# Kernel optimization log

Measured on AMD Instinct MI355X. Metric: run time of the kernel, lower is better.

Reference implementation:

```python
import jax, jax.numpy as jnp
import numpy as np

B, S, D, E, HD, F, L, CYCLES = 2, 1024, 1000, 20, 50, 2048, 14, 3


def setup_inputs() -> dict:
    key = jax.random.key(0)
    k = jax.random.split(key, 8)
    sc = 0.02
    return {
        "x": jax.random.normal(k[0], (B, S, D), jnp.float32),
        "expert_w": jax.random.normal(k[1], (L, E, D, 3 * HD), jnp.float32) * sc,
        "expert_b": jnp.zeros((L, E, 3 * HD), jnp.float32),
        "router_w": jax.random.normal(k[2], (L, D, E), jnp.float32) * sc,
        "router_b": jnp.zeros((L, E), jnp.float32),
        "out_w": jax.random.normal(k[3], (L, D, D), jnp.float32) * sc,
        "out_b": jnp.zeros((L, D), jnp.float32),
        "ln1_g": jnp.ones((L, D), jnp.float32),
        "ln1_b": jnp.zeros((L, D), jnp.float32),
        "ff_w1": jax.random.normal(k[4], (L, D, F), jnp.float32) * sc,
        "ff_b1": jnp.zeros((L, F), jnp.float32),
        "ff_w2": jax.random.normal(k[5], (L, F, D), jnp.float32) * sc,
        "ff_b2": jnp.zeros((L, D), jnp.float32),
        "ln2_g": jnp.ones((L, D), jnp.float32),
        "ln2_b": jnp.zeros((L, D), jnp.float32),
    }


def _layer_norm(x, g, b):
    m = jnp.mean(x, -1, keepdims=True)
    v = jnp.mean((x - m) ** 2, -1, keepdims=True)
    return (x - m) * jax.lax.rsqrt(v + 1e-5) * g + b


def _moe_attn(x, ew, eb, rw, rb, ow, ob):
    # x: [b, s, d]; ew: [E, d, 3*HD]; routing softmax over experts
    b_, s_, d_ = x.shape
    routing = jax.nn.softmax(x @ rw + rb, axis=-1)           # [b, s, E]
    qkv = jnp.einsum('bsd,edh->besh', x, ew) + eb[None, :, None, :]
    q, k, v = jnp.split(qkv, 3, axis=-1)                     # each [b, E, s, HD]
    scores = jnp.einsum('besh,beth->best', q, k) * (HD ** -0.5)
    attn = jax.nn.softmax(scores, axis=-1)
    out = jnp.einsum('best,beth->besh', attn, v)             # [b, E, s, HD]
    out = out * jnp.transpose(routing, (0, 2, 1))[..., None]
    # disjoint head slices -> reshape is exactly the torch slice-add combine
    out = jnp.transpose(out, (0, 2, 1, 3)).reshape(b_, s_, d_)
    return out @ ow + ob


def _block(x, i, p):
    a = _moe_attn(x, p['expert_w'][i], p['expert_b'][i], p['router_w'][i],
                  p['router_b'][i], p['out_w'][i], p['out_b'][i])
    x = _layer_norm(x + a, p['ln1_g'][i], p['ln1_b'][i])
    h = jax.nn.gelu(x @ p['ff_w1'][i] + p['ff_b1'][i], approximate=False)
    f = h @ p['ff_w2'][i] + p['ff_b2'][i]
    return _layer_norm(x + f, p['ln2_g'][i], p['ln2_b'][i])


def _slam(x, p):
    s = x.shape[1]
    x = _block(x, 0, p)
    bounds = [(0, min(int(s * 0.45), s)),
              (max(int(s * 0.25), 0), min(int(s * 0.65), s)),
              (max(int(s * 0.45), 0), min(int(s * 0.85), s)),
              (max(int(s * 0.65), 0), s)]
    wrap = max(min(int(s * 0.05), s // 10), 1) if s > 20 else 0
    counts = np.zeros(s, np.float32)
    for st, en in bounds:
        counts[st:en] += 1.0
    if wrap:
        counts[:wrap] += 1.0
    counts = jnp.asarray(np.maximum(counts, 1.0))[None, :, None]
    for c in range(CYCLES):
        x_new = jnp.zeros_like(x)
        for j, (st, en) in enumerate(bounds):
            li = 1 + 4 * c + j
            if j == 3 and wrap:
                seg = jnp.concatenate([x[:, st:s], x[:, :wrap]], axis=1)
                out = _block(seg, li, p)
                x_new = x_new.at[:, st:s].add(out[:, :s - st])
                x_new = x_new.at[:, :wrap].add(out[:, s - st:])
            else:
                out = _block(x[:, st:en], li, p)
                x_new = x_new.at[:, st:en].add(out)
        x = x_new / counts
    return _block(x, L - 1, p)


def reference(x, expert_w, expert_b, router_w, router_b, out_w, out_b,
              ln1_g, ln1_b, ff_w1, ff_b1, ff_w2, ff_b2, ln2_g, ln2_b):
    p = dict(expert_w=expert_w, expert_b=expert_b, router_w=router_w,
             router_b=router_b, out_w=out_w, out_b=out_b, ln1_g=ln1_g,
             ln1_b=ln1_b, ff_w1=ff_w1, ff_b1=ff_b1, ff_w2=ff_w2,
             ff_b2=ff_b2, ln2_g=ln2_g, ln2_b=ln2_b)
    return _slam(x, p)
```

## Files before the change

kernel.cpp:

```cpp
#include <hip/hip_runtime.h>
#include <math.h>

namespace {

constexpr int kB  = 2;
constexpr int kS  = 1024;
constexpr int kD  = 1000;
constexpr int kE  = 20;
constexpr int kHD = 50;
constexpr int kF  = 2048;
constexpr int kQKV = 3 * kHD;

__global__ __launch_bounds__(256) void zero_kernel(float* __restrict__ p, int n) {
    int i = blockIdx.x * 256 + threadIdx.x;
    if (i < n) p[i] = 0.0f;
}

__global__ __launch_bounds__(256) void gelu_kernel(float* __restrict__ p, int n) {
    int i = blockIdx.x * 256 + threadIdx.x;
    if (i < n) {
        float x = p[i];
        p[i] = 0.5f * x * (1.0f + erff(x * 0.70710678118654752440f));
    }
}

__global__ __launch_bounds__(256) void init_bias_kernel(float* __restrict__ C,
                                                        const float* __restrict__ bias,
                                                        long long total, int N) {
    long long i = (long long)blockIdx.x * 256 + threadIdx.x;
    if (i < total) C[i] = bias[(int)(i % N)];
}

__global__ __launch_bounds__(256) void gather_kernel(const float* __restrict__ src,
                                                     float* __restrict__ dst,
                                                     int st, int sseg) {
    int i = blockIdx.x * 256 + threadIdx.x;
    int tot = kB * sseg * kD;
    if (i >= tot) return;
    int d  = i % kD;
    int tr = i / kD;
    int r  = tr % sseg;
    int b  = tr / sseg;
    int srow = st + r;
    if (srow >= kS) srow -= kS;
    dst[i] = src[(b * kS + srow) * kD + d];
}

__global__ __launch_bounds__(256) void scatter_add_kernel(const float* __restrict__ src,
                                                          float* __restrict__ dst,
                                                          int st, int sseg) {
    int i = blockIdx.x * 256 + threadIdx.x;
    int tot = kB * sseg * kD;
    if (i >= tot) return;
    int d  = i % kD;
    int tr = i / kD;
    int r  = tr % sseg;
    int b  = tr / sseg;
    int drow = st + r;
    if (drow >= kS) drow -= kS;
    dst[(b * kS + drow) * kD + d] += src[i];
}

__global__ __launch_bounds__(256) void finalize_kernel(const float* __restrict__ xn,
                                                       float* __restrict__ cur) {
    int i = blockIdx.x * 256 + threadIdx.x;
    const int tot = kB * kS * kD;
    if (i >= tot) return;
    int r = (i / kD) % kS;
    float cnt = 0.0f;
    cnt += (r < 460) ? 1.0f : 0.0f;
    cnt += (r >= 256 && r < 665) ? 1.0f : 0.0f;
    cnt += (r >= 460 && r < 870) ? 1.0f : 0.0f;
    cnt += (r >= 665) ? 1.0f : 0.0f;
    cnt += (r < 51) ? 1.0f : 0.0f;
    cnt = fmaxf(cnt, 1.0f);
    cur[i] = xn[i] / cnt;
}

template<int BM, int BN, int TM, int TN, int NMAP, bool ATOMIC>
__global__ __launch_bounds__(256) void gemm_tile(
    const float* __restrict__ A, const float* __restrict__ W,
    const float* __restrict__ bias, float* __restrict__ C,
    int M, int N, int K, int kchunk,
    long long strideW, long long strideC, long long strideBias)
{
    constexpr int BK = 16;
    constexpr int TX = BN / TN;
    constexpr int TY = BM / TM;
    static_assert(TX * TY == 256, "block must be 256 threads");
    static_assert(TM % 4 == 0 && TN % 4 == 0, "vector frags");

    int kbeg = 0, kend = K;
    if (ATOMIC) {
        kbeg = blockIdx.z * kchunk;
        kend = min(K, kbeg + kchunk);
    } else {
        W    += (long long)blockIdx.z * strideW;
        C    += (long long)blockIdx.z * strideC;
        bias += (long long)blockIdx.z * strideBias;
    }

    __shared__ __align__(16) float As[BK][BM + 4];
    __shared__ __align__(16) float Bs[BK][BN];

    const int tid  = threadIdx.x;
    const int tx   = tid % TX;
    const int ty   = tid / TX;
    const int row0 = blockIdx.y * BM;
    const int col0 = blockIdx.x * BN;

    float acc[TM][TN] = {};

    for (int k0 = kbeg; k0 < kend; k0 += BK) {
        #pragma unroll
        for (int i = 0; i < BM / 64; i++) {
            int f  = tid + i * 256;
            int r  = f >> 2;
            int cv = f & 3;
            int gr = row0 + r;
            int gc = k0 + cv * 4;
            float4 av = make_float4(0.f, 0.f, 0.f, 0.f);
            if (gr < M) {
                if (gc + 3 < kend) {
                    av = *reinterpret_cast<const float4*>(A + (long long)gr * K + gc);
                } else {
                    float t0 = (gc + 0 < kend) ? A[(long long)gr * K + gc + 0] : 0.f;
                    float t1 = (gc + 1 < kend) ? A[(long long)gr * K + gc + 1] : 0.f;
                    float t2 = (gc + 2 < kend) ? A[(long long)gr * K + gc + 2] : 0.f;
                    float t3 = (gc + 3 < kend) ? A[(long long)gr * K + gc + 3] : 0.f;
                    av = make_float4(t0, t1, t2, t3);
                }
            }
            As[cv * 4 + 0][r] = av.x;
            As[cv * 4 + 1][r] = av.y;
            As[cv * 4 + 2][r] = av.z;
            As[cv * 4 + 3][r] = av.w;
        }

        if (NMAP > 0) {
            #pragma unroll
            for (int it = 0; it < (BK * BN) / 256; it++) {
                int idx = tid + it * 256;
                int r = idx / BN, c = idx % BN;
                int gr = k0 + r, gc = col0 + c;
                float v = 0.f;
                if (gr < kend && gc < N) {
                    int e = gc / NMAP;
                    int n = gc - e * NMAP;
                    v = W[(long long)e * K * NMAP + (long long)gr * NMAP + n];
                }
                Bs[r][c] = v;
            }
        } else {
            #pragma unroll
            for (int i = 0; i < BN / 64; i++) {
                int f  = tid + i * 256;
                int r  = f / (BN / 4);
                int cv = f % (BN / 4);
                int gr = k0 + r;
                int gc = col0 + cv * 4;
                float4 bv = make_float4(0.f, 0.f, 0.f, 0.f);
                if (gr < kend) {
                    if (gc + 3 < N) {
                        bv = *reinterpret_cast<const float4*>(W + (long long)gr * N + gc);
                    } else {
                        float t0 = (gc + 0 < N) ? W[(long long)gr * N + gc + 0] : 0.f;
                        float t1 = (gc + 1 < N) ? W[(long long)gr * N + gc + 1] : 0.f;
                        float t2 = (gc + 2 < N) ? W[(long long)gr * N + gc + 2] : 0.f;
                        float t3 = (gc + 3 < N) ? W[(long long)gr * N + gc + 3] : 0.f;
                        bv = make_float4(t0, t1, t2, t3);
                    }
                }
                *reinterpret_cast<float4*>(&Bs[r][cv * 4]) = bv;
            }
        }
        __syncthreads();

        #pragma unroll
        for (int kk = 0; kk < BK; kk++) {
            float a[TM], b[TN];
            #pragma unroll
            for (int i = 0; i < TM; i += 4) {
                float4 v = *reinterpret_cast<const float4*>(&As[kk][ty * TM + i]);
                a[i] = v.x; a[i + 1] = v.y; a[i + 2] = v.z; a[i + 3] = v.w;
            }
            #pragma unroll
            for (int j = 0; j < TN; j += 4) {
                float4 v = *reinterpret_cast<const float4*>(&Bs[kk][tx * TN + j]);
                b[j] = v.x; b[j + 1] = v.y; b[j + 2] = v.z; b[j + 3] = v.w;
            }
            #pragma unroll
            for (int i = 0; i < TM; i++)
                #pragma unroll
                for (int j = 0; j < TN; j++)
                    acc[i][j] = fmaf(a[i], b[j], acc[i][j]);
        }
        __syncthreads();
    }

    #pragma unroll
    for (int i = 0; i < TM; i++) {
        int gr = row0 + ty * TM + i;
        if (gr >= M) continue;
        if (ATOMIC) {
            #pragma unroll
            for (int j = 0; j < TN; j++) {
                int gc = col0 + tx * TN + j;
                if (gc < N) atomicAdd(&C[(long long)gr * N + gc], acc[i][j]);
            }
        } else if (NMAP > 0) {
            #pragma unroll
            for (int j = 0; j < TN; j++) {
                int gc = col0 + tx * TN + j;
                if (gc < N) {
                    int e = gc / NMAP;
                    int n = gc - e * NMAP;
                    C[(long long)e * M * NMAP + (long long)gr * NMAP + n] =
                        acc[i][j] + bias[gc];
                }
            }
        } else {
            #pragma unroll
            for (int j = 0; j < TN; j += 4) {
                int gc = col0 + tx * TN + j;
                if (gc + 3 < N) {
                    float4 bv = *reinterpret_cast<const float4*>(bias + gc);
                    float4 o  = make_float4(acc[i][j + 0] + bv.x,
                                            acc[i][j + 1] + bv.y,
                                            acc[i][j + 2] + bv.z,
                                            acc[i][j + 3] + bv.w);
                    *reinterpret_cast<float4*>(C + (long long)gr * N + gc) = o;
                } else {
                    for (int jj = 0; jj < 4; jj++) {
                        int g = gc + jj;
                        if (g < N) C[(long long)gr * N + g] = acc[i][j + jj] + bias[g];
                    }
                }
            }
        }
    }
}

inline int pick_split(int gx, int gy, int K) {
    int blocks = gx * gy;
    int S = (512 + blocks - 1) / blocks;
    if (S < 1) S = 1;
    if (S > 4) S = 4;
    while (S > 1 && (K + S - 1) / S < 64) S--;
    return S;
}

inline void gemm_auto(const float* A, const float* W, const float* bias, float* C,
                      int M, int N, int K, hipStream_t stream)
{
    constexpr int BM = 128, BN = 64, TM = 8, TN = 4;
    int gx = (N + BN - 1) / BN, gy = (M + BM - 1) / BM;
    int S = pick_split(gx, gy, K);
    if (S == 1) {
        dim3 grid(gx, gy, 1);
        gemm_tile<BM, BN, TM, TN, 0, false><<<grid, 256, 0, stream>>>(
            A, W, bias, C, M, N, K, K, 0, 0, 0);
    } else {
        long long total = (long long)M * N;
        init_bias_kernel<<<(unsigned)((total + 255) / 256), 256, 0, stream>>>(
            C, bias, total, N);
        int Kc = ((K + S - 1) / S + 15) & ~15;
        dim3 grid(gx, gy, S);
        gemm_tile<BM, BN, TM, TN, 0, true><<<grid, 256, 0, stream>>>(
            A, W, nullptr, C, M, N, K, Kc, 0, 0, 0);
    }
}

__global__ __launch_bounds__(256) void routing_kernel(
    const float* __restrict__ X, const float* __restrict__ RW,
    const float* __restrict__ RB, float* __restrict__ R, int T)
{
    int wave = (blockIdx.x * 256 + threadIdx.x) / 64;
    int lane = threadIdx.x & 63;
    if (wave >= T) return;
    const float* x = X + (long long)wave * kD;

    float xr[16];
    #pragma unroll
    for (int i = 0; i < 16; i++) {
        int d = lane + 64 * i;
        xr[i] = (d < kD) ? x[d] : 0.0f;
    }
    float r[kE];
    #pragma unroll
    for (int e = 0; e < kE; e++) {
        float acc = 0.0f;
        #pragma unroll
        for (int i = 0; i < 16; i++) {
            int d = lane + 64 * i;
            if (d < kD) acc = fmaf(xr[i], RW[d * kE + e], acc);
        }
        #pragma unroll
        for (int off = 32; off > 0; off >>= 1) acc += __shfl_xor(acc, off, 64);
        r[e] = acc + RB[e];
    }
    float m = r[0];
    #pragma unroll
    for (int e = 1; e < kE; e++) m = fmaxf(m, r[e]);
    float sum = 0.0f;
    #pragma unroll
    for (int e = 0; e < kE; e++) { r[e] = expf(r[e] - m); sum += r[e]; }
    float inv = 1.0f / sum;
    float mine = 0.0f;
    #pragma unroll
    for (int e = 0; e < kE; e++) if (lane == e) mine = r[e] * inv;
    if (lane < kE) R[(long long)wave * kE + lane] = mine;
}

constexpr int QT_STR = 68;
constexpr int VS_STR = 52;
constexpr int SB_STR = 68;

__global__ __launch_bounds__(256) void attn_kernel(
    const float* __restrict__ QKV, const float* __restrict__ R,
    float* __restrict__ O, int s)
{
    const int q0 = blockIdx.x * 64;
    const int e  = blockIdx.y;
    const int b  = blockIdx.z;
    const int T  = kB * s;
    const float* base = QKV + ((long long)e * T + (long long)b * s) * kQKV;

    __shared__ __align__(16) float Qt[kHD * QT_STR];
    __shared__ __align__(16) float Vs[64 * VS_STR];
    __shared__ __align__(16) float KS[64 * SB_STR];

    const int tid = threadIdx.x;
    const int tx  = tid & 15;
    const int ty  = tid >> 4;
    const int row = ty * 4;

    for (int idx = tid; idx < 64 * kHD; idx += 256) {
        int r = idx / kHD, h = idx % kHD;
        int q = q0 + r;
        Qt[h * QT_STR + r] = (q < s) ? base[(long long)q * kQKV + h] : 0.0f;
    }

    float o[4][4] = {};
    float m[4] = {-1e30f, -1e30f, -1e30f, -1e30f};
    float l[4] = {};

    const int ntile = (s + 63) / 64;
    for (int t = 0; t < ntile; t++) {
        const int k0 = t * 64;
        const int kn = min(64, s - k0);

        __syncthreads();
        for (int idx = tid; idx < 64 * kHD; idx += 256) {
            int r = idx / kHD, h = idx % kHD;
            const float* rowp = base + (long long)(k0 + r) * kQKV;
            bool ok = (r < kn);
            KS[h * SB_STR + r]  = ok ? rowp[kHD + h] : 0.0f;
            Vs[r * VS_STR + h]  = ok ? rowp[2 * kHD + h] : 0.0f;
        }
        __syncthreads();

        float sacc[4][4] = {};
        #pragma unroll 2
        for (int kk = 0; kk < kHD; kk++) {
            float4 a4 = *reinterpret_cast<const float4*>(&Qt[kk * QT_STR + row]);
            float4 b4 = *reinterpret_cast<const float4*>(&KS[kk * SB_STR + tx * 4]);
            const float av[4] = {a4.x, a4.y, a4.z, a4.w};
            const float bv[4] = {b4.x, b4.y, b4.z, b4.w};
            #pragma unroll
            for (int i = 0; i < 4; i++)
                #pragma unroll
                for (int j = 0; j < 4; j++)
                    sacc[i][j] = fmaf(av[i], bv[j], sacc[i][j]);
        }

        #pragma unroll
        for (int i = 0; i < 4; i++) {
            #pragma unroll
            for (int j = 0; j < 4; j++) {
                float v = sacc[i][j] * 0.14142135623730950488f;
                sacc[i][j] = (tx * 4 + j < kn) ? v : -1e30f;
            }
            float rm = fmaxf(fmaxf(sacc[i][0], sacc[i][1]),
                             fmaxf(sacc[i][2], sacc[i][3]));
            rm = fmaxf(rm, __shfl_xor(rm, 1, 64));
            rm = fmaxf(rm, __shfl_xor(rm, 2, 64));
            rm = fmaxf(rm, __shfl_xor(rm, 4, 64));
            rm = fmaxf(rm, __shfl_xor(rm, 8, 64));
            float mn = fmaxf(m[i], rm);
            float alpha = __expf(m[i] - mn);
            m[i] = mn;
            float rs = 0.0f;
            #pragma unroll
            for (int j = 0; j < 4; j++) {
                float p = __expf(sacc[i][j] - mn);
                sacc[i][j] = p;
                rs += p;
            }
            rs += __shfl_xor(rs, 1, 64);
            rs += __shfl_xor(rs, 2, 64);
            rs += __shfl_xor(rs, 4, 64);
            rs += __shfl_xor(rs, 8, 64);
            l[i] = l[i] * alpha + rs;
            #pragma unroll
            for (int c = 0; c < 4; c++) o[i][c] *= alpha;
        }

        __syncthreads();
        #pragma unroll
        for (int i = 0; i < 4; i++)
            *reinterpret_cast<float4*>(&KS[(row + i) * SB_STR + tx * 4]) =
                make_float4(sacc[i][0], sacc[i][1], sacc[i][2], sacc[i][3]);
        __syncthreads();

        #pragma unroll 2
        for (int j0 = 0; j0 < 64; j0 += 4) {
            float4 pr[4], vr[4];
            #pragma unroll
            for (int i = 0; i < 4; i++)
                pr[i] = *reinterpret_cast<const float4*>(&KS[(row + i) * SB_STR + j0]);
            #pragma unroll
            for (int jj = 0; jj < 4; jj++)
                vr[jj] = *reinterpret_cast<const float4*>(&Vs[(j0 + jj) * VS_STR + tx * 4]);
            #pragma unroll
            for (int i = 0; i < 4; i++) {
                const float pv[4] = {pr[i].x, pr[i].y, pr[i].z, pr[i].w};
                #pragma unroll
                for (int jj = 0; jj < 4; jj++) {
                    o[i][0] = fmaf(pv[jj], vr[jj].x, o[i][0]);
                    o[i][1] = fmaf(pv[jj], vr[jj].y, o[i][1]);
                    o[i][2] = fmaf(pv[jj], vr[jj].z, o[i][2]);
                    o[i][3] = fmaf(pv[jj], vr[jj].w, o[i][3]);
                }
            }
        }
    }

    const int hbase = tx * 4;
    if (hbase < kHD) {
        #pragma unroll
        for (int i = 0; i < 4; i++) {
            int q = q0 + row + i;
            if (q >= s) continue;
            long long tok = (long long)b * s + q;
            float sc = R[tok * kE + e] / l[i];
            float* op = O + tok * kD + e * kHD + hbase;
            if (hbase + 3 < kHD) {
                *reinterpret_cast<float2*>(op) =
                    make_float2(o[i][0] * sc, o[i][1] * sc);
                *reinterpret_cast<float2*>(op + 2) =
                    make_float2(o[i][2] * sc, o[i][3] * sc);
            } else {
                op[0] = o[i][0] * sc;
                op[1] = o[i][1] * sc;
            }
        }
    }
}

__global__ __launch_bounds__(256) void ln_kernel(
    const float* __restrict__ Xres, const float* __restrict__ A,
    const float* __restrict__ G, const float* __restrict__ Bb,
    float* __restrict__ Y)
{
    const int t = blockIdx.x;
    const float* x = Xres + (long long)t * kD;
    const float* a = A + (long long)t * kD;
    __shared__ float buf[kD];
    __shared__ float red[4];
    const int tid = threadIdx.x;

    float lsum = 0.0f;
    for (int d = tid; d < kD; d += 256) {
        float v = x[d] + a[d];
        buf[d] = v;
        lsum += v;
    }
    #pragma unroll
    for (int off = 32; off > 0; off >>= 1) lsum += __shfl_xor(lsum, off, 64);
    if ((tid & 63) == 0) red[tid >> 6] = lsum;
    __syncthreads();
    float mean = (red[0] + red[1] + red[2] + red[3]) * (1.0f / kD);

    float lv = 0.0f;
    for (int d = tid; d < kD; d += 256) {
        float u = buf[d] - mean;
        lv = fmaf(u, u, lv);
    }
    #pragma unroll
    for (int off = 32; off > 0; off >>= 1) lv += __shfl_xor(lv, off, 64);
    __syncthreads();
    if ((tid & 63) == 0) red[tid >> 6] = lv;
    __syncthreads();
    float var = (red[0] + red[1] + red[2] + red[3]) * (1.0f / kD);
    float inv = rsqrtf(var + 1e-5f);

    for (int d = tid; d < kD; d += 256)
        Y[(long long)t * kD + d] = (buf[d] - mean) * inv * G[d] + Bb[d];
}

struct Params {
    const float *expert_w, *expert_b, *router_w, *router_b, *out_w, *out_b;
    const float *ln1_g, *ln1_b, *ff_w1, *ff_b1, *ff_w2, *ff_b2, *ln2_g, *ln2_b;
};

void run_block(const float* xin, float* xout, int s, int li, const Params& P,
               float* routing, float* qkv, float* attn_comb, float* a_out,
               float* y1, float* h, float* f, hipStream_t stream)
{
    const int T = kB * s;

    routing_kernel<<<(T + 3) / 4, 256, 0, stream>>>(
        xin, P.router_w + (long long)li * kD * kE, P.router_b + li * kE, routing, T);

    {
        dim3 grid((kE * kQKV + 63) / 64, (T + 127) / 128, 1);
        gemm_tile<128, 64, 8, 4, kQKV, false><<<grid, 256, 0, stream>>>(
            xin, P.expert_w + (long long)li * kE * kD * kQKV,
            P.expert_b + (long long)li * kE * kQKV, qkv,
            T, kE * kQKV, kD, kD, 0, 0, 0);
    }

    {
        dim3 grid((s + 63) / 64, kE, kB);
        attn_kernel<<<grid, 256, 0, stream>>>(qkv, routing, attn_comb, s);
    }

    gemm_auto(attn_comb, P.out_w + (long long)li * kD * kD,
              P.out_b + li * kD, a_out, T, kD, kD, stream);

    ln_kernel<<<T, 256, 0, stream>>>(xin, a_out, P.ln1_g + li * kD, P.ln1_b + li * kD, y1);

    gemm_auto(y1, P.ff_w1 + (long long)li * kD * kF,
              P.ff_b1 + li * kF, h, T, kF, kD, stream);

    gelu_kernel<<<(T * kF + 255) / 256, 256, 0, stream>>>(h, T * kF);

    gemm_auto(h, P.ff_w2 + (long long)li * kF * kD,
              P.ff_b2 + li * kD, f, T, kD, kF, stream);

    ln_kernel<<<T, 256, 0, stream>>>(y1, f, P.ln2_g + li * kD, P.ln2_b + li * kD, xout);
}

}

extern "C" void kernel_launch(void* const* d_in, const int* in_sizes, int n_in,
                              void* d_out, int out_size, void* d_ws, size_t ws_size,
                              hipStream_t stream)
{
    const float* x = (const float*)d_in[0];
    Params P;
    P.expert_w = (const float*)d_in[1];
    P.expert_b = (const float*)d_in[2];
    P.router_w = (const float*)d_in[3];
    P.router_b = (const float*)d_in[4];
    P.out_w    = (const float*)d_in[5];
    P.out_b    = (const float*)d_in[6];
    P.ln1_g    = (const float*)d_in[7];
    P.ln1_b    = (const float*)d_in[8];
    P.ff_w1    = (const float*)d_in[9];
    P.ff_b1    = (const float*)d_in[10];
    P.ff_w2    = (const float*)d_in[11];
    P.ff_b2    = (const float*)d_in[12];
    P.ln2_g    = (const float*)d_in[13];
    P.ln2_b    = (const float*)d_in[14];

    const int TD = kB * kS * kD;
    float* ws = (float*)d_ws;
    float* cur       = ws;  ws += TD;
    float* xnew      = ws;  ws += TD;
    float* seg       = ws;  ws += TD;
    float* routing   = ws;  ws += kB * kS * kE;
    float* qkv       = ws;  ws += kE * kB * kS * kQKV;
    float* attn_comb = ws;  ws += TD;
    float* a_out     = ws;  ws += TD;
    float* y1        = ws;  ws += TD;
    float* h         = ws;  ws += kB * kS * kF;
    float* f         = ws;  ws += TD;
    float* bout      = (float*)d_out;

    run_block(x, cur, kS, 0, P, routing, qkv, attn_comb, a_out, y1, h, f, stream);

    const int st_arr[4]  = {0, 256, 460, 665};
    const int len_arr[4] = {460, 409, 410, 410};

    for (int c = 0; c < 3; c++) {
        zero_kernel<<<(TD + 255) / 256, 256, 0, stream>>>(xnew, TD);
        for (int j = 0; j < 4; j++) {
            const int st = st_arr[j], sl = len_arr[j];
            const int li = 1 + 4 * c + j;
            const int n = kB * sl * kD;
            gather_kernel<<<(n + 255) / 256, 256, 0, stream>>>(cur, seg, st, sl);
            run_block(seg, bout, sl, li, P, routing, qkv, attn_comb, a_out, y1, h, f, stream);
            scatter_add_kernel<<<(n + 255) / 256, 256, 0, stream>>>(bout, xnew, st, sl);
        }
        finalize_kernel<<<(TD + 255) / 256, 256, 0, stream>>>(xnew, cur);
    }

    run_block(cur, (float*)d_out, kS, 13, P, routing, qkv, attn_comb, a_out, y1, h, f, stream);
}
```

Measured before the change: 10.56 ms.

## Double-buffer GEMM tiles, add 128x128 tile path, fuse GELU into FF1 epilogue

Rewrites the fp32 tiled GEMM to prefetch the next K-tile into registers and store it into a second shared-memory buffer while the current one is computed, so each K-step needs one barrier instead of two. The per-thread fragment is split into strided 4-wide groups to reduce LDS bank conflicts. A 128x128 tile variant is used when the grid is large enough, and the split-K heuristic is retuned. GELU is applied in the FF1 GEMM epilogue instead of a separate pass. In exchange, shared memory and register use go up, which may lower occupancy.

```diff
diff --git a/kernel.cpp b/kernel.cpp
--- a/kernel.cpp
+++ b/kernel.cpp
@@ -77,31 +77,27 @@
     cur[i] = xn[i] / cnt;
 }
 
-template<int BM, int BN, int TM, int TN, int NMAP, bool ATOMIC>
+template<int BM, int BN, int TM, int TN, int NMAP, bool ATOMIC, bool GELU>
 __global__ __launch_bounds__(256) void gemm_tile(
     const float* __restrict__ A, const float* __restrict__ W,
     const float* __restrict__ bias, float* __restrict__ C,
-    int M, int N, int K, int kchunk,
-    long long strideW, long long strideC, long long strideBias)
-{
-    constexpr int BK = 16;
-    constexpr int TX = BN / TN;
-    constexpr int TY = BM / TM;
+    int M, int N, int K, int kchunk)
+{
+    constexpr int BK  = 16;
+    constexpr int NGM = TM / 4;
+    constexpr int NGN = TN / 4;
+    constexpr int TX  = BN / TN;
+    constexpr int TY  = BM / TM;
     static_assert(TX * TY == 256, "block must be 256 threads");
-    static_assert(TM % 4 == 0 && TN % 4 == 0, "vector frags");
 
     int kbeg = 0, kend = K;
-    if (ATOMIC) {
+    if constexpr (ATOMIC) {
         kbeg = blockIdx.z * kchunk;
         kend = min(K, kbeg + kchunk);
-    } else {
-        W    += (long long)blockIdx.z * strideW;
-        C    += (long long)blockIdx.z * strideC;
-        bias += (long long)blockIdx.z * strideBias;
-    }
-
-    __shared__ __align__(16) float As[BK][BM + 4];
-    __shared__ __align__(16) float Bs[BK][BN];
+    }
+
+    __shared__ __align__(16) float As[2][BK][BM + 4];
+    __shared__ __align__(16) float Bs[2][BK][BN];
 
     const int tid  = threadIdx.x;
     const int tx   = tid % TX;
@@ -109,11 +105,19 @@
     const int row0 = blockIdx.y * BM;
     const int col0 = blockIdx.x * BN;
 
-    float acc[TM][TN] = {};
-
-    for (int k0 = kbeg; k0 < kend; k0 += BK) {
-        #pragma unroll
-        for (int i = 0; i < BM / 64; i++) {
+    constexpr int AV  = BM / 64;
+    constexpr int BV  = (NMAP == 0) ? BN / 64 : 1;
+    constexpr int BSC = (NMAP > 0) ? (BK * BN / 256) : 1;
+
+    float4 areg[AV];
+    float4 breg[BV];
+    float  bsc[BSC];
+
+    float acc[NGM][4][NGN][4] = {};
+
+    auto loadg = [&](int k0) {
+        #pragma unroll
+        for (int i = 0; i < AV; i++) {
             int f  = tid + i * 256;
             int r  = f >> 2;
             int cv = f & 3;
@@ -124,23 +128,18 @@
                 if (gc + 3 < kend) {
                     av = *reinterpret_cast<const float4*>(A + (long long)gr * K + gc);
                 } else {
-                    float t0 = (gc + 0 < kend) ? A[(long long)gr * K + gc + 0] : 0.f;
-                    float t1 = (gc + 1 < kend) ? A[(long long)gr * K + gc + 1] : 0.f;
-                    float t2 = (gc + 2 < kend) ? A[(long long)gr * K + gc + 2] : 0.f;
-                    float t3 = (gc + 3 < kend) ? A[(long long)gr * K + gc + 3] : 0.f;
-                    av = make_float4(t0, t1, t2, t3);
+                    av.x = (gc + 0 < kend) ? A[(long long)gr * K + gc + 0] : 0.f;
+                    av.y = (gc + 1 < kend) ? A[(long long)gr * K + gc + 1] : 0.f;
+                    av.z = (gc + 2 < kend) ? A[(long long)gr * K + gc + 2] : 0.f;
+                    av.w = (gc + 3 < kend) ? A[(long long)gr * K + gc + 3] : 0.f;
                 }
             }
-            As[cv * 4 + 0][r] = av.x;
-            As[cv * 4 + 1][r] = av.y;
-            As[cv * 4 + 2][r] = av.z;
-            As[cv * 4 + 3][r] = av.w;
-        }
-
-        if (NMAP > 0) {
-            #pragma unroll
-            for (int it = 0; it < (BK * BN) / 256; it++) {
-                int idx = tid + it * 256;
+            areg[i] = av;
+        }
+        if constexpr (NMAP > 0) {
+            #pragma unroll
+            for (int i = 0; i < BSC; i++) {
+                int idx = tid + i * 256;
                 int r = idx / BN, c = idx % BN;
                 int gr = k0 + r, gc = col0 + c;
                 float v = 0.f;
@@ -149,11 +148,11 @@
                     int n = gc - e * NMAP;
                     v = W[(long long)e * K * NMAP + (long long)gr * NMAP + n];
                 }
-                Bs[r][c] = v;
+                bsc[i] = v;
             }
         } else {
             #pragma unroll
-            for (int i = 0; i < BN / 64; i++) {
+            for (int i = 0; i < BV; i++) {
                 int f  = tid + i * 256;
                 int r  = f / (BN / 4);
                 int cv = f % (BN / 4);
@@ -164,76 +163,135 @@
                     if (gc + 3 < N) {
                         bv = *reinterpret_cast<const float4*>(W + (long long)gr * N + gc);
                     } else {
-                        float t0 = (gc + 0 < N) ? W[(long long)gr * N + gc + 0] : 0.f;
-                        float t1 = (gc + 1 < N) ? W[(long long)gr * N + gc + 1] : 0.f;
-                        float t2 = (gc + 2 < N) ? W[(long long)gr * N + gc + 2] : 0.f;
-                        float t3 = (gc + 3 < N) ? W[(long long)gr * N + gc + 3] : 0.f;
-                        bv = make_float4(t0, t1, t2, t3);
+                        bv.x = (gc + 0 < N) ? W[(long long)gr * N + gc + 0] : 0.f;
+                        bv.y = (gc + 1 < N) ? W[(long long)gr * N + gc + 1] : 0.f;
+                        bv.z = (gc + 2 < N) ? W[(long long)gr * N + gc + 2] : 0.f;
+                        bv.w = (gc + 3 < N) ? W[(long long)gr * N + gc + 3] : 0.f;
                     }
                 }
-                *reinterpret_cast<float4*>(&Bs[r][cv * 4]) = bv;
-            }
-        }
-        __syncthreads();
-
+                breg[i] = bv;
+            }
+        }
+    };
+
+    auto stlds = [&](int buf) {
+        #pragma unroll
+        for (int i = 0; i < AV; i++) {
+            int f  = tid + i * 256;
+            int r  = f >> 2;
+            int cv = f & 3;
+            As[buf][cv * 4 + 0][r] = areg[i].x;
+            As[buf][cv * 4 + 1][r] = areg[i].y;
+            As[buf][cv * 4 + 2][r] = areg[i].z;
+            As[buf][cv * 4 + 3][r] = areg[i].w;
+        }
+        if constexpr (NMAP > 0) {
+            #pragma unroll
+            for (int i = 0; i < BSC; i++) {
+                int idx = tid + i * 256;
+                Bs[buf][idx / BN][idx % BN] = bsc[i];
+            }
+        } else {
+            #pragma unroll
+            for (int i = 0; i < BV; i++) {
+                int f  = tid + i * 256;
+                *reinterpret_cast<float4*>(&Bs[buf][f / (BN / 4)][(f % (BN / 4)) * 4]) = breg[i];
+            }
+        }
+    };
+
+    auto compute = [&](int buf) {
         #pragma unroll
         for (int kk = 0; kk < BK; kk++) {
-            float a[TM], b[TN];
-            #pragma unroll
-            for (int i = 0; i < TM; i += 4) {
-                float4 v = *reinterpret_cast<const float4*>(&As[kk][ty * TM + i]);
-                a[i] = v.x; a[i + 1] = v.y; a[i + 2] = v.z; a[i + 3] = v.w;
-            }
-            #pragma unroll
-            for (int j = 0; j < TN; j += 4) {
-                float4 v = *reinterpret_cast<const float4*>(&Bs[kk][tx * TN + j]);
-                b[j] = v.x; b[j + 1] = v.y; b[j + 2] = v.z; b[j + 3] = v.w;
-            }
-            #pragma unroll
-            for (int i = 0; i < TM; i++)
+            float a[NGM][4], b[NGN][4];
+            #pragma unroll
+            for (int g = 0; g < NGM; g++) {
+                float4 v = *reinterpret_cast<const float4*>(&As[buf][kk][ty * 4 + g * (BM / 2)]);
+                a[g][0] = v.x; a[g][1] = v.y; a[g][2] = v.z; a[g][3] = v.w;
+            }
+            #pragma unroll
+            for (int h2 = 0; h2 < NGN; h2++) {
+                float4 v = *reinterpret_cast<const float4*>(&Bs[buf][kk][tx * 4 + h2 * (BN / 2)]);
+                b[h2][0] = v.x; b[h2][1] = v.y; b[h2][2] = v.z; b[h2][3] = v.w;
+            }
+            #pragma unroll
+            for (int g = 0; g < NGM; g++)
                 #pragma unroll
-                for (int j = 0; j < TN; j++)
-                    acc[i][j] = fmaf(a[i], b[j], acc[i][j]);
-        }
-        __syncthreads();
-    }
-
-    #pragma unroll
-    for (int i = 0; i < TM; i++) {
-        int gr = row0 + ty * TM + i;
-        if (gr >= M) continue;
-        if (ATOMIC) {
-            #pragma unroll
-            for (int j = 0; j < TN; j++) {
-                int gc = col0 + tx * TN + j;
-                if (gc < N) atomicAdd(&C[(long long)gr * N + gc], acc[i][j]);
-            }
-        } else if (NMAP > 0) {
-            #pragma unroll
-            for (int j = 0; j < TN; j++) {
-                int gc = col0 + tx * TN + j;
-                if (gc < N) {
-                    int e = gc / NMAP;
-                    int n = gc - e * NMAP;
-                    C[(long long)e * M * NMAP + (long long)gr * NMAP + n] =
-                        acc[i][j] + bias[gc];
-                }
-            }
-        } else {
-            #pragma unroll
-            for (int j = 0; j < TN; j += 4) {
-                int gc = col0 + tx * TN + j;
-                if (gc + 3 < N) {
-                    float4 bv = *reinterpret_cast<const float4*>(bias + gc);
-                    float4 o  = make_float4(acc[i][j + 0] + bv.x,
-                                            acc[i][j + 1] + bv.y,
-                                            acc[i][j + 2] + bv.z,
-                                            acc[i][j + 3] + bv.w);
-                    *reinterpret_cast<float4*>(C + (long long)gr * N + gc) = o;
+                for (int i = 0; i < 4; i++)
+                    #pragma unroll
+                    for (int h2 = 0; h2 < NGN; h2++)
+                        #pragma unroll
+                        for (int j = 0; j < 4; j++)
+                            acc[g][i][h2][j] = fmaf(a[g][i], b[h2][j], acc[g][i][h2][j]);
+        }
+    };
+
+    const int nt = (kend - kbeg + BK - 1) / BK;
+    loadg(kbeg);
+    stlds(0);
+    __syncthreads();
+    for (int t = 0; t < nt; t++) {
+        const int cur = t & 1;
+        if (t + 1 < nt) loadg(kbeg + (t + 1) * BK);
+        compute(cur);
+        if (t + 1 < nt) {
+            stlds(cur ^ 1);
+            __syncthreads();
+        }
+    }
+
+    #pragma unroll
+    for (int g = 0; g < NGM; g++) {
+        #pragma unroll
+        for (int i = 0; i < 4; i++) {
+            int gr = row0 + ty * 4 + g * (BM / 2) + i;
+            if (gr >= M) continue;
+            #pragma unroll
+            for (int h2 = 0; h2 < NGN; h2++) {
+                int gc0 = col0 + tx * 4 + h2 * (BN / 2);
+                if constexpr (ATOMIC) {
+                    #pragma unroll
+                    for (int j = 0; j < 4; j++) {
+                        int gc = gc0 + j;
+                        if (gc < N) atomicAdd(&C[(long long)gr * N + gc], acc[g][i][h2][j]);
+                    }
+                } else if constexpr (NMAP > 0) {
+                    #pragma unroll
+                    for (int j = 0; j < 4; j++) {
+                        int gc = gc0 + j;
+                        if (gc < N) {
+                            int e = gc / NMAP;
+                            int n = gc - e * NMAP;
+                            C[(long long)e * M * NMAP + (long long)gr * NMAP + n] =
+                                acc[g][i][h2][j] + bias[gc];
+                        }
+                    }
                 } else {
-                    for (int jj = 0; jj < 4; jj++) {
-                        int g = gc + jj;
-                        if (g < N) C[(long long)gr * N + g] = acc[i][j + jj] + bias[g];
+                    if (gc0 + 3 < N) {
+                        float4 bv = *reinterpret_cast<const float4*>(bias + gc0);
+                        float v0 = acc[g][i][h2][0] + bv.x;
+                        float v1 = acc[g][i][h2][1] + bv.y;
+                        float v2 = acc[g][i][h2][2] + bv.z;
+                        float v3 = acc[g][i][h2][3] + bv.w;
+                        if constexpr (GELU) {
+                            v0 = 0.5f * v0 * (1.0f + erff(v0 * 0.70710678118654752440f));
+                            v1 = 0.5f * v1 * (1.0f + erff(v1 * 0.70710678118654752440f));
+                            v2 = 0.5f * v2 * (1.0f + erff(v2 * 0.70710678118654752440f));
+                            v3 = 0.5f * v3 * (1.0f + erff(v3 * 0.70710678118654752440f));
+                        }
+                        *reinterpret_cast<float4*>(C + (long long)gr * N + gc0) =
+                            make_float4(v0, v1, v2, v3);
+                    } else {
+                        #pragma unroll
+                        for (int j = 0; j < 4; j++) {
+                            int gc = gc0 + j;
+                            if (gc < N) {
+                                float v = acc[g][i][h2][j] + bias[gc];
+                                if constexpr (GELU)
+                                    v = 0.5f * v * (1.0f + erff(v * 0.70710678118654752440f));
+                                C[(long long)gr * N + gc] = v;
+                            }
+                        }
                     }
                 }
             }
@@ -241,33 +299,64 @@
     }
 }
 
-inline int pick_split(int gx, int gy, int K) {
+inline void gemm_auto(const float* A, const float* W, const float* bias, float* C,
+                      int M, int N, int K, bool gelu, hipStream_t stream)
+{
+    int gx1 = (N + 127) / 128, gy1 = (M + 127) / 128;
+    if (gx1 * gy1 >= 256) {
+        dim3 grid(gx1, gy1, 1);
+        if (gelu)
+            gemm_tile<128, 128, 8, 8, 0, false, true><<<grid, 256, 0, stream>>>(
+                A, W, bias, C, M, N, K, K);
+        else
+            gemm_tile<128, 128, 8, 8, 0, false, false><<<grid, 256, 0, stream>>>(
+                A, W, bias, C, M, N, K, K);
+        return;
+    }
+    int gx = (N + 63) / 64, gy = (M + 127) / 128;
     int blocks = gx * gy;
-    int S = (512 + blocks - 1) / blocks;
-    if (S < 1) S = 1;
-    if (S > 4) S = 4;
-    while (S > 1 && (K + S - 1) / S < 64) S--;
-    return S;
-}
-
-inline void gemm_auto(const float* A, const float* W, const float* bias, float* C,
-                      int M, int N, int K, hipStream_t stream)
-{
-    constexpr int BM = 128, BN = 64, TM = 8, TN = 4;
-    int gx = (N + BN - 1) / BN, gy = (M + BM - 1) / BM;
-    int S = pick_split(gx, gy, K);
-    if (S == 1) {
+    int S = 1;
+    if (blocks < 224) {
+        S = (384 + blocks - 1) / blocks;
+        if (S > 4) S = 4;
+        while (S > 1 && (K + S - 1) / S < 128) S--;
+    }
+    if (S <= 1) {
         dim3 grid(gx, gy, 1);
-        gemm_tile<BM, BN, TM, TN, 0, false><<<grid, 256, 0, stream>>>(
-            A, W, bias, C, M, N, K, K, 0, 0, 0);
+        if (gelu)
+            gemm_tile<128, 64, 8, 4, 0, false, true><<<grid, 256, 0, stream>>>(
+                A, W, bias, C, M, N, K, K);
+        else
+            gemm_tile<128, 64, 8, 4, 0, false, false><<<grid, 256, 0, stream>>>(
+                A, W, bias, C, M, N, K, K);
     } else {
         long long total = (long long)M * N;
         init_bias_kernel<<<(unsigned)((total + 255) / 256), 256, 0, stream>>>(
             C, bias, total, N);
-        int Kc = ((K + S - 1) / S + 15) & ~15;
+        int Kc = (((K + S - 1) / S) + 15) & ~15;
         dim3 grid(gx, gy, S);
-        gemm_tile<BM, BN, TM, TN, 0, true><<<grid, 256, 0, stream>>>(
-            A, W, nullptr, C, M, N, K, Kc, 0, 0, 0);
+        gemm_tile<128, 64, 8, 4, 0, true, false><<<grid, 256, 0, stream>>>(
+            A, W, nullptr, C, M, N, K, Kc);
+        if (gelu)
+            gelu_kernel<<<(unsigned)((total + 255) / 256), 256, 0, stream>>>(C, (int)total);
+    }
+}
+
+inline void qkv_auto(const float* A, const float* W, const float* bias, float* C,
+                     int M, hipStream_t stream)
+{
+    const int N = kE * kQKV;
+    int gy = (M + 127) / 128;
+    int gx1 = (N + 127) / 128;
+    if (gx1 * gy >= 256) {
+        dim3 grid(gx1, gy, 1);
+        gemm_tile<128, 128, 8, 8, kQKV, false, false><<<grid, 256, 0, stream>>>(
+            A, W, bias, C, M, N, kD, kD);
+    } else {
+        int gx = (N + 63) / 64;
+        dim3 grid(gx, gy, 1);
+        gemm_tile<128, 64, 8, 4, kQKV, false, false><<<grid, 256, 0, stream>>>(
+            A, W, bias, C, M, N, kD, kD);
     }
 }
 
@@ -513,13 +602,8 @@
     routing_kernel<<<(T + 3) / 4, 256, 0, stream>>>(
         xin, P.router_w + (long long)li * kD * kE, P.router_b + li * kE, routing, T);
 
-    {
-        dim3 grid((kE * kQKV + 63) / 64, (T + 127) / 128, 1);
-        gemm_tile<128, 64, 8, 4, kQKV, false><<<grid, 256, 0, stream>>>(
-            xin, P.expert_w + (long long)li * kE * kD * kQKV,
-            P.expert_b + (long long)li * kE * kQKV, qkv,
-            T, kE * kQKV, kD, kD, 0, 0, 0);
-    }
+    qkv_auto(xin, P.expert_w + (long long)li * kE * kD * kQKV,
+             P.expert_b + (long long)li * kE * kQKV, qkv, T, stream);
 
     {
         dim3 grid((s + 63) / 64, kE, kB);
@@ -527,17 +611,15 @@
     }
 
     gemm_auto(attn_comb, P.out_w + (long long)li * kD * kD,
-              P.out_b + li * kD, a_out, T, kD, kD, stream);
+              P.out_b + li * kD, a_out, T, kD, kD, false, stream);
 
     ln_kernel<<<T, 256, 0, stream>>>(xin, a_out, P.ln1_g + li * kD, P.ln1_b + li * kD, y1);
 
     gemm_auto(y1, P.ff_w1 + (long long)li * kD * kF,
-              P.ff_b1 + li * kF, h, T, kF, kD, stream);
-
-    gelu_kernel<<<(T * kF + 255) / 256, 256, 0, stream>>>(h, T * kF);
+              P.ff_b1 + li * kF, h, T, kF, kD, true, stream);
 
     gemm_auto(h, P.ff_w2 + (long long)li * kF * kD,
-              P.ff_b2 + li * kD, f, T, kD, kF, stream);
+              P.ff_b2 + li * kD, f, T, kD, kF, false, stream);
 
     ln_kernel<<<T, 256, 0, stream>>>(y1, f, P.ln2_g + li * kD, P.ln2_b + li * kD, xout);
 }
```

Result: slower. 11.44 ms (+8.4%).
